# Kernel optimization log

Measured on AMD Instinct MI355X. Metric: run time of the kernel, lower is better.

Reference implementation:

```python
import jax, jax.numpy as jnp
import numpy as np

NB_CLS, NB_QRY, NB_SHOT, FEAT_DIM = 5, 75, 5, 640
Q_STEPS, LR_DNI, HID = 3, 1e-3, 4096
N = NB_CLS + NB_QRY           # nodes in similarity graph (80)
M = 1 + N                     # subgraph size (81)
# strict upper triangle of MxM minus the query-query block (matches triu_index_input)
_t = np.ones((M, M)); _t[1 + NB_CLS:, 1 + NB_CLS:] = 0
_t = np.triu(_t, 1)
MASK_IDX = jnp.asarray(np.flatnonzero(_t.ravel() == 1))
DNI_IN = int(MASK_IDX.shape[0])  # 465


def _pairwise(supp, query):
    feat = jnp.concatenate([supp, query], 0)
    nrm = jnp.maximum(jnp.linalg.norm(feat, axis=-1, keepdims=True), 1e-12)
    feat = feat / nrm
    sim = feat @ feat.T                      # (N, N)
    sim_ss = sim[:NB_CLS, :NB_CLS]
    sim_qq = sim[NB_CLS:, NB_CLS:]
    sim_sq = sim[:NB_CLS, NB_CLS:]
    sim_feat_support = jnp.concatenate([sim_ss, sim_sq], 1).T   # (N, nb_cls)
    sim_feat_query = jnp.concatenate([sim_sq, sim_qq], 0)       # (N, nb_qry)
    return sim_feat_support, sim_feat_query, sim_sq


def _subgraph(sim_s, sim_q):
    # topk indices are constants wrt grad (no_grad in torch; ints in jax)
    idx_q = jax.lax.top_k(sim_q, NB_QRY)[1] + NB_CLS
    idx_s = jax.lax.top_k(sim_s, NB_CLS)[1]
    index = jnp.concatenate([jnp.arange(N, dtype=idx_s.dtype)[:, None], idx_s, idx_q], 1)  # (N, M)
    sim = jnp.concatenate([sim_s, sim_q], 1)                     # (N, N)
    sub = sim[index[:, :, None], index[:, None, :]]              # (N, M, M) batched gather
    return sub.reshape(N, M * M)[:, MASK_IDX]                    # (N, DNI_IN)


def _dni(x, W1, b1, W2, b2, W3, b3):
    h = jax.nn.relu(x @ W1.T + b1)
    h = jax.nn.relu(h @ W2.T + b2)
    return h @ W3.T + b3


def _refine(supp, query, ds, dq):
    for _ in range(Q_STEPS):
        inputs, vjp = jax.vjp(lambda s: _subgraph(*_pairwise(s, query)[:2]), supp)
        supp = supp - LR_DNI * vjp(_dni(inputs, *ds))[0]
        inputs, vjp = jax.vjp(lambda q: _subgraph(*_pairwise(supp, q)[:2]), query)
        query = query - LR_DNI * vjp(_dni(inputs, *dq))[0]
    return supp, query


def setup_inputs() -> dict:
    key = jax.random.key(0)
    ks = jax.random.split(key, 16)
    d = {
        "feat_support": jax.random.normal(ks[0], (NB_CLS, NB_SHOT, FEAT_DIM), jnp.float32),
        "feat_query": jax.random.normal(ks[1], (NB_QRY, FEAT_DIM), jnp.float32),
        "scale_cls": jnp.full((1,), 10.0, jnp.float32),
    }
    names = ["ds_W1", "ds_b1", "ds_W2", "ds_b2", "ds_W3", "ds_b3",
             "dq_W1", "dq_b1", "dq_W2", "dq_b2", "dq_W3", "dq_b3"]
    shapes = [(HID, DNI_IN), (HID,), (HID, HID), (HID,), (DNI_IN, HID), (DNI_IN,)] * 2
    for i, (n, sh) in enumerate(zip(names, shapes)):
        d[n] = jax.random.normal(ks[2 + i], sh, jnp.float32) * 0.02
    return d


def reference(feat_support, feat_query, scale_cls,
              ds_W1, ds_b1, ds_W2, ds_b2, ds_W3, ds_b3,
              dq_W1, dq_b1, dq_W2, dq_b2, dq_W3, dq_b3):
    supp = feat_support.mean(1)                                  # (nb_cls, feat_dim)
    ds = (ds_W1, ds_b1, ds_W2, ds_b2, ds_W3, ds_b3)
    dq = (dq_W1, dq_b1, dq_W2, dq_b2, dq_W3, dq_b3)
    supp, query = _refine(supp, feat_query, ds, dq)
    _, _, sim_sq = _pairwise(supp, query)
    return (sim_sq * scale_cls).T                                # (nb_qry, nb_cls)
```

## Files before the change

kernel.cpp:

```cpp
#include <hip/hip_runtime.h>

#define NCLS 5
#define NQRY 75
#define NTOT 80
#define FD   640
#define HIDN 4096
#define DNIN 465
#define KPAD 512
#define NPAD 512
#define LRDNI 1e-3f

typedef short  v8s __attribute__((ext_vector_type(8)));
typedef float  v4f __attribute__((ext_vector_type(4)));

__device__ __forceinline__ ushort f2bf(float x) {
    uint u = __float_as_uint(x);
    u = (u + 0x7FFFu + ((u >> 16) & 1u)) >> 16;
    return (ushort)u;
}
__device__ __forceinline__ uint pk2(float a, float b) {
    return (uint)f2bf(a) | ((uint)f2bf(b) << 16);
}

__global__ __launch_bounds__(256) void k_setup(
                        const float* __restrict__ fs, const float* __restrict__ fq,
                        const float* __restrict__ W1s, const float* __restrict__ W1q,
                        const float* __restrict__ W2s, const float* __restrict__ W2q,
                        const float* __restrict__ W3s, const float* __restrict__ W3q,
                        ushort* __restrict__ W1bs, ushort* __restrict__ W1bq,
                        ushort* __restrict__ W2bs, ushort* __restrict__ W2bq,
                        ushort* __restrict__ W3bs, ushort* __restrict__ W3bq,
                        float* __restrict__ supp, float* __restrict__ qbuf) {
    int tid = blockIdx.x * 256 + threadIdx.x;

    #pragma unroll
    for (int i = 0; i < 4; i++) {
        int oo = tid + i * 524288;
        int l = oo & 63, ks = (oo >> 6) & 127, nt = oo >> 13;
        int n = nt * 16 + (l & 15), kb = ks * 32 + ((l >> 4) << 3);
        size_t src = (size_t)n * HIDN + kb;
        float4 s0 = *(const float4*)(W2s + src);
        float4 s1 = *(const float4*)(W2s + src + 4);
        float4 t0 = *(const float4*)(W2q + src);
        float4 t1 = *(const float4*)(W2q + src + 4);
        uint4 qa, qb;
        qa.x = pk2(s0.x, s0.y); qa.y = pk2(s0.z, s0.w);
        qa.z = pk2(s1.x, s1.y); qa.w = pk2(s1.z, s1.w);
        qb.x = pk2(t0.x, t0.y); qb.y = pk2(t0.z, t0.w);
        qb.z = pk2(t1.x, t1.y); qb.w = pk2(t1.z, t1.w);
        *(uint4*)(W2bs + (size_t)oo * 8) = qa;
        *(uint4*)(W2bq + (size_t)oo * 8) = qb;
    }

    {
        int oo = tid & 262143;
        const float* Ws = (tid < 262144) ? W1s : W1q;
        ushort* Wd = (tid < 262144) ? W1bs : W1bq;
        int l = oo & 63, ks = (oo >> 6) & 15, nt = oo >> 10;
        int n = nt * 16 + (l & 15), kb = ks * 32 + ((l >> 4) << 3);
        ushort tmp[8];
        #pragma unroll
        for (int j = 0; j < 8; j++) {
            int k = kb + j;
            tmp[j] = (k < DNIN) ? f2bf(Ws[n * DNIN + k]) : (ushort)0;
        }
        *(uint4*)(Wd + (size_t)oo * 8) = *(uint4*)tmp;
    }

    {
        int oo = tid & 262143;
        const float* Ws = (tid < 262144) ? W3s : W3q;
        ushort* Wd = (tid < 262144) ? W3bs : W3bq;
        int l = oo & 63, ks = (oo >> 6) & 127, nt = oo >> 13;
        int n = nt * 16 + (l & 15), kb = ks * 32 + ((l >> 4) << 3);
        uint4 q;
        if (n < DNIN) {
            float4 f0 = *(const float4*)(Ws + (size_t)n * HIDN + kb);
            float4 f1 = *(const float4*)(Ws + (size_t)n * HIDN + kb + 4);
            q.x = pk2(f0.x, f0.y); q.y = pk2(f0.z, f0.w);
            q.z = pk2(f1.x, f1.y); q.w = pk2(f1.z, f1.w);
        } else q = (uint4){0, 0, 0, 0};
        *(uint4*)(Wd + (size_t)oo * 8) = q;
    }

    if (tid < NCLS * FD) {
        int c = tid / FD, d = tid % FD;
        float s = 0.f;
        #pragma unroll
        for (int t = 0; t < 5; t++) s += fs[(c * 5 + t) * FD + d];
        supp[tid] = s * 0.2f;
    }
    if (tid < NQRY * FD / 4)
        ((float4*)qbuf)[tid] = ((const float4*)fq)[tid];
}

__device__ __forceinline__ const float* rowptr(const float* supp, const float* qbuf, int r) {
    return (r < NCLS) ? (supp + r * FD) : (qbuf + (r - NCLS) * FD);
}

template<bool FIN>
__global__ void k_simrank(const float* __restrict__ supp, const float* __restrict__ qbuf,
                          float* __restrict__ f, float* __restrict__ nrm,
                          float* __restrict__ S, int* __restrict__ perm,
                          const float* __restrict__ scale, float* __restrict__ out) {
    __shared__ float fi[FD];
    __shared__ float row[NTOT];
    __shared__ float ssh[NTOT];
    int i = blockIdx.x;
    int t = threadIdx.x;
    const float* ri = rowptr(supp, qbuf, i);
    for (int u = t; u < FD; u += 128) fi[u] = ri[u];
    __syncthreads();
    float dot = 0.f;
    if (t < NTOT) {
        const float* rj = rowptr(supp, qbuf, t);
        float ss = 0.f;
        for (int k = 0; k < FD; k += 4) {
            float4 a = *(const float4*)(fi + k);
            float4 b = *(const float4*)(rj + k);
            dot += a.x * b.x + a.y * b.y + a.z * b.z + a.w * b.w;
            ss  += b.x * b.x + b.y * b.y + b.z * b.z + b.w * b.w;
        }
        ssh[t] = ss;
    }
    __syncthreads();
    float ni = fmaxf(sqrtf(ssh[i]), 1e-12f);
    float inv_i = 1.0f / ni;
    if (t < NTOT) {
        float nt = fmaxf(sqrtf(ssh[t]), 1e-12f);
        float val = dot * inv_i / nt;
        if (FIN) {
            if (t >= NCLS) out[(t - NCLS) * NCLS + i] = val * scale[0];
        } else {
            row[t] = val;
            S[i * NTOT + t] = val;
        }
    }
    if (FIN) return;
    __syncthreads();
    for (int u = t; u < FD; u += 128) f[i * FD + u] = fi[u] * inv_i;
    if (t == 0) { nrm[i] = ni; perm[i * 81] = i; }
    if (t < NCLS) {
        float v = row[t]; int rank = 0;
        for (int k = 0; k < NCLS; k++) {
            float w = row[k];
            if (w > v || (w == v && k < t)) rank++;
        }
        perm[i * 81 + 1 + rank] = t;
    } else if (t < NTOT) {
        int j = t - NCLS; float v = row[t]; int rank = 0;
        for (int k = NCLS; k < NTOT; k++) {
            float w = row[k];
            if (w > v || (w == v && (k - NCLS) < j)) rank++;
        }
        perm[i * 81 + 6 + rank] = t;
    }
}

__device__ __forceinline__ void mask_ab(int m, int& a, int& b) {
    int start = 0, len = 80, aa = 0;
    while (m >= start + len) { start += len; len--; aa++; }
    a = aa; b = aa + 1 + (m - start);
}

__global__ void k_gather(const float* __restrict__ S, const int* __restrict__ perm,
                         ushort* __restrict__ Xb, float* __restrict__ Gs) {
    __shared__ int p[81];
    int i = blockIdx.x;
    int t = threadIdx.x;
    if (t < 81) p[t] = perm[i * 81 + t];
    if (t < NTOT) Gs[i * NTOT + t] = 0.f;
    __syncthreads();
    if (t < DNIN) {
        int a, b; mask_ab(t, a, b);
        Xb[i * KPAD + t] = f2bf(S[p[a] * NTOT + p[b]]);
    } else if (t < KPAD) {
        Xb[i * KPAD + t] = 0;
    }
}

template<int WAVES, int KPW, bool EPI>
__global__ __launch_bounds__(WAVES * 64) void k_gemmws(
        const ushort* __restrict__ A, int lda,
        const ushort* __restrict__ Bf, int nks,
        const float* __restrict__ bias, ushort* __restrict__ H,
        float* __restrict__ C, int ldcp) {
    __shared__ v4f red[WAVES][5][64];
    int t = threadIdx.x;
    int w = t >> 6, lane = t & 63, l16 = lane & 15, quad = lane >> 4;
    int n0 = blockIdx.x * 16;
    int kc0 = w * (KPW * 32);
    const ushort* Ap = A + l16 * lda + kc0 + quad * 8;
    const ushort* Bp = Bf + ((size_t)blockIdx.x * nks + (kc0 >> 5)) * 512 + lane * 8;

    v4f acc[5];
    #pragma unroll
    for (int mt = 0; mt < 5; mt++) acc[mt] = (v4f){0.f, 0.f, 0.f, 0.f};

    #pragma unroll
    for (int s = 0; s < KPW; s++) {
        v8s a[5], b;
        #pragma unroll
        for (int mt = 0; mt < 5; mt++)
            a[mt] = *(const v8s*)(Ap + mt * 16 * lda + s * 32);
        b = *(const v8s*)(Bp + (size_t)s * 512);
        #pragma unroll
        for (int mt = 0; mt < 5; mt++)
            acc[mt] = __builtin_amdgcn_mfma_f32_16x16x32_bf16(a[mt], b, acc[mt], 0, 0, 0);
    }
    #pragma unroll
    for (int mt = 0; mt < 5; mt++) red[w][mt][lane] = acc[mt];
    __syncthreads();

    #pragma unroll
    for (int j = 0; j < (1280 + WAVES * 64 - 1) / (WAVES * 64); j++) {
        int row = j * (WAVES * 4) + (t >> 4);
        if (row < 80) {
            int col = t & 15;
            int mt = row >> 4, rr = row & 15, qq = rr >> 2, r = rr & 3;
            int ln = qq * 16 + col;
            float v = 0.f;
            #pragma unroll
            for (int w2 = 0; w2 < WAVES; w2++) v += red[w2][mt][ln][r];
            if (EPI) {
                v += bias[n0 + col];
                H[(size_t)row * HIDN + n0 + col] = f2bf(fmaxf(v, 0.f));
            } else {
                C[(size_t)row * ldcp + n0 + col] = v;
            }
        }
    }
}

__global__ void k_scatter(const float* __restrict__ P3, const float* __restrict__ b3,
                          const int* __restrict__ perm, float* __restrict__ Gs) {
    __shared__ int p[81];
    int i = blockIdx.x;
    int t = threadIdx.x;
    if (t < 81) p[t] = perm[i * 81 + t];
    __syncthreads();
    if (t < DNIN) {
        float g = b3[t] + P3[i * NPAD + t];
        int a, b; mask_ab(t, a, b);
        atomicAdd(&Gs[p[a] * NTOT + p[b]], g);
    }
}

__global__ void k_bwd(const float* __restrict__ Gs, const float* __restrict__ f,
                      const float* __restrict__ nrm, float* __restrict__ target,
                      int row0) {
    int r = row0 + blockIdx.x;
    __shared__ float cj[NTOT];
    __shared__ float red[2];
    int t = threadIdx.x;
    if (t < NTOT) cj[t] = Gs[r * NTOT + t] + Gs[t * NTOT + r];
    __syncthreads();
    float df[5] = {0.f, 0.f, 0.f, 0.f, 0.f};
    for (int j = 0; j < NTOT; j++) {
        float c = cj[j];
        const float* fj = f + j * FD;
        #pragma unroll
        for (int u = 0; u < 5; u++) df[u] += c * fj[t + 128 * u];
    }
    const float* fr = f + r * FD;
    float frv[5]; float partial = 0.f;
    #pragma unroll
    for (int u = 0; u < 5; u++) { frv[u] = fr[t + 128 * u]; partial += df[u] * frv[u]; }
    #pragma unroll
    for (int o = 32; o > 0; o >>= 1) partial += __shfl_xor(partial, o, 64);
    if ((t & 63) == 0) red[t >> 6] = partial;
    __syncthreads();
    float dot = red[0] + red[1];
    float invn = 1.0f / nrm[r];
    float* dst = target + blockIdx.x * FD;
    #pragma unroll
    for (int u = 0; u < 5; u++) {
        float dx = (df[u] - dot * frv[u]) * invn;
        dst[t + 128 * u] -= LRDNI * dx;
    }
}

extern "C" void kernel_launch(void* const* d_in, const int* in_sizes, int n_in,
                              void* d_out, int out_size, void* d_ws, size_t ws_size,
                              hipStream_t stream) {
    const float* fs    = (const float*)d_in[0];
    const float* fq    = (const float*)d_in[1];
    const float* scale = (const float*)d_in[2];
    const float* W[12];
    for (int i = 0; i < 12; i++) W[i] = (const float*)d_in[3 + i];

    float* base = (float*)d_ws;
    float* supp = base;
    float* qbuf = supp + 3200;
    float* f    = qbuf + 48000;
    float* nrm  = f + 51200;
    float* S    = nrm + 96;
    int*   perm = (int*)(S + 6400);
    float* P3   = (float*)(perm + 6496);
    float* Gs   = P3 + 80 * NPAD;
    ushort* Xb  = (ushort*)(Gs + 6400);
    ushort* H1b = Xb + 80 * KPAD;
    ushort* H2b = H1b + 80 * HIDN;
    ushort* W1b_ds = H2b + 80 * HIDN;
    ushort* W1b_dq = W1b_ds + HIDN * KPAD;
    ushort* W3b_ds = W1b_dq + HIDN * KPAD;
    ushort* W3b_dq = W3b_ds + NPAD * HIDN;
    ushort* W2b_ds = W3b_dq + NPAD * HIDN;
    ushort* W2b_dq = W2b_ds + (size_t)HIDN * HIDN;

    k_setup<<<2048, 256, 0, stream>>>(fs, fq, W[0], W[6], W[2], W[8], W[4], W[10],
                                      W1b_ds, W1b_dq, W2b_ds, W2b_dq, W3b_ds, W3b_dq,
                                      supp, qbuf);

    for (int step = 0; step < 3; step++) {
        for (int half = 0; half < 2; half++) {
            const float* const* w = (half == 0) ? W : (W + 6);
            const ushort* W1b = (half == 0) ? W1b_ds : W1b_dq;
            const ushort* W2b = (half == 0) ? W2b_ds : W2b_dq;
            const ushort* W3b = (half == 0) ? W3b_ds : W3b_dq;
            k_simrank<false><<<80, 128, 0, stream>>>(supp, qbuf, f, nrm, S, perm, nullptr, nullptr);
            k_gather<<<80, 512, 0, stream>>>(S, perm, Xb, Gs);
            k_gemmws<4, 4, true><<<256, 256, 0, stream>>>(
                Xb, KPAD, W1b, 16, w[1], H1b, nullptr, 0);
            k_gemmws<4, 32, true><<<256, 256, 0, stream>>>(
                H1b, HIDN, W2b, 128, w[3], H2b, nullptr, 0);
            k_gemmws<8, 16, false><<<32, 512, 0, stream>>>(
                H2b, HIDN, W3b, 128, nullptr, nullptr, P3, NPAD);
            k_scatter<<<80, 512, 0, stream>>>(P3, w[5], perm, Gs);
            if (half == 0) k_bwd<<<5, 128, 0, stream>>>(Gs, f, nrm, supp, 0);
            else           k_bwd<<<75, 128, 0, stream>>>(Gs, f, nrm, qbuf, NCLS);
        }
    }
    k_simrank<true><<<5, 128, 0, stream>>>(supp, qbuf, f, nrm, S, perm, scale, (float*)d_out);
}
```

Before: 731.8 us.

## Split-K third DNI GEMM across 256 blocks with atomics; widen first two GEMMs

The third DNI layer GEMM (80x4096 by 4096x512) previously ran on only 32 blocks. It is now split along K into 32 chunks across an 8x32 grid, and partial results are combined with float atomicAdd into P3. P3 is zeroed in the gather kernel for this. The first two GEMMs move from 4 to 8 waves per block with half the K per wave, which adds intra-block split-K parallelism. The aim is better CU occupancy on the memory-bound weight streaming, at the cost of atomic traffic and nondeterministic summation order.

```diff
diff --git a/kernel.cpp b/kernel.cpp
--- a/kernel.cpp
+++ b/kernel.cpp
@@ -164,12 +164,14 @@
 }
 
 __global__ void k_gather(const float* __restrict__ S, const int* __restrict__ perm,
-                         ushort* __restrict__ Xb, float* __restrict__ Gs) {
+                         ushort* __restrict__ Xb, float* __restrict__ Gs,
+                         float* __restrict__ P3) {
     __shared__ int p[81];
     int i = blockIdx.x;
     int t = threadIdx.x;
     if (t < 81) p[t] = perm[i * 81 + t];
     if (t < NTOT) Gs[i * NTOT + t] = 0.f;
+    P3[i * NPAD + t] = 0.f;
     __syncthreads();
     if (t < DNIN) {
         int a, b; mask_ab(t, a, b);
@@ -179,13 +181,12 @@
     }
 }
 
-template<int WAVES, int KPW, bool EPI>
-__global__ __launch_bounds__(WAVES * 64) void k_gemmws(
+template<int KPW>
+__global__ __launch_bounds__(512) void k_gemmws(
         const ushort* __restrict__ A, int lda,
         const ushort* __restrict__ Bf, int nks,
-        const float* __restrict__ bias, ushort* __restrict__ H,
-        float* __restrict__ C, int ldcp) {
-    __shared__ v4f red[WAVES][5][64];
+        const float* __restrict__ bias, ushort* __restrict__ H) {
+    __shared__ v4f red[8][5][64];
     int t = threadIdx.x;
     int w = t >> 6, lane = t & 63, l16 = lane & 15, quad = lane >> 4;
     int n0 = blockIdx.x * 16;
@@ -213,23 +214,53 @@
     __syncthreads();
 
     #pragma unroll
-    for (int j = 0; j < (1280 + WAVES * 64 - 1) / (WAVES * 64); j++) {
-        int row = j * (WAVES * 4) + (t >> 4);
+    for (int j = 0; j < 3; j++) {
+        int row = j * 32 + (t >> 4);
         if (row < 80) {
             int col = t & 15;
             int mt = row >> 4, rr = row & 15, qq = rr >> 2, r = rr & 3;
             int ln = qq * 16 + col;
             float v = 0.f;
             #pragma unroll
-            for (int w2 = 0; w2 < WAVES; w2++) v += red[w2][mt][ln][r];
-            if (EPI) {
-                v += bias[n0 + col];
-                H[(size_t)row * HIDN + n0 + col] = f2bf(fmaxf(v, 0.f));
-            } else {
-                C[(size_t)row * ldcp + n0 + col] = v;
-            }
-        }
-    }
+            for (int w2 = 0; w2 < 8; w2++) v += red[w2][mt][ln][r];
+            v += bias[n0 + col];
+            H[(size_t)row * HIDN + n0 + col] = f2bf(fmaxf(v, 0.f));
+        }
+    }
+}
+
+__global__ __launch_bounds__(256) void k_gemm3(
+        const ushort* __restrict__ A, int lda,
+        const ushort* __restrict__ Bf, int nks,
+        float* __restrict__ P3) {
+    int tid = threadIdx.x;
+    int w = tid >> 6, lane = tid & 63, l16 = lane & 15, quad = lane >> 4;
+    int n0 = blockIdx.x * 64 + w * 16;
+    int kc0 = blockIdx.y * 128;
+    const ushort* Ap = A + l16 * lda + kc0 + quad * 8;
+    const ushort* Bp = Bf + ((size_t)(n0 >> 4) * nks + (kc0 >> 5)) * 512 + lane * 8;
+
+    v4f acc[5];
+    #pragma unroll
+    for (int mt = 0; mt < 5; mt++) acc[mt] = (v4f){0.f, 0.f, 0.f, 0.f};
+
+    #pragma unroll
+    for (int s = 0; s < 4; s++) {
+        v8s a[5], b;
+        #pragma unroll
+        for (int mt = 0; mt < 5; mt++)
+            a[mt] = *(const v8s*)(Ap + mt * 16 * lda + s * 32);
+        b = *(const v8s*)(Bp + (size_t)s * 512);
+        #pragma unroll
+        for (int mt = 0; mt < 5; mt++)
+            acc[mt] = __builtin_amdgcn_mfma_f32_16x16x32_bf16(a[mt], b, acc[mt], 0, 0, 0);
+    }
+    int col = n0 + l16;
+    #pragma unroll
+    for (int mt = 0; mt < 5; mt++)
+        #pragma unroll
+        for (int r = 0; r < 4; r++)
+            atomicAdd(&P3[(mt * 16 + quad * 4 + r) * NPAD + col], acc[mt][r]);
 }
 
 __global__ void k_scatter(const float* __restrict__ P3, const float* __restrict__ b3,
@@ -319,13 +350,10 @@
             const ushort* W2b = (half == 0) ? W2b_ds : W2b_dq;
             const ushort* W3b = (half == 0) ? W3b_ds : W3b_dq;
             k_simrank<false><<<80, 128, 0, stream>>>(supp, qbuf, f, nrm, S, perm, nullptr, nullptr);
-            k_gather<<<80, 512, 0, stream>>>(S, perm, Xb, Gs);
-            k_gemmws<4, 4, true><<<256, 256, 0, stream>>>(
-                Xb, KPAD, W1b, 16, w[1], H1b, nullptr, 0);
-            k_gemmws<4, 32, true><<<256, 256, 0, stream>>>(
-                H1b, HIDN, W2b, 128, w[3], H2b, nullptr, 0);
-            k_gemmws<8, 16, false><<<32, 512, 0, stream>>>(
-                H2b, HIDN, W3b, 128, nullptr, nullptr, P3, NPAD);
+            k_gather<<<80, 512, 0, stream>>>(S, perm, Xb, Gs, P3);
+            k_gemmws<2><<<256, 512, 0, stream>>>(Xb, KPAD, W1b, 16, w[1], H1b);
+            k_gemmws<16><<<256, 512, 0, stream>>>(H1b, HIDN, W2b, 128, w[3], H2b);
+            k_gemm3<<<dim3(8, 32), 256, 0, stream>>>(H2b, HIDN, W3b, 128, P3);
             k_scatter<<<80, 512, 0, stream>>>(P3, w[5], perm, Gs);
             if (half == 0) k_bwd<<<5, 128, 0, stream>>>(Gs, f, nrm, supp, 0);
             else           k_bwd<<<75, 128, 0, stream>>>(Gs, f, nrm, qbuf, NCLS);
```

Measured after the change: 638.8 us. -12.7%, faster.
